# Performance work log

Measured on AMD Instinct MI355X. Metric: run time of the kernel, lower is better.

The kernel has to match this reference:

```python
import jax, jax.numpy as jnp
import numpy as np

PRE_HEIGHT = 96
PRE_WIDTH = 128


def setup_inputs() -> dict:
    key = jax.random.key(0)
    B, K, H, W = 32, 64, 96, 128
    x = jax.random.normal(key, (B, K, H, W), dtype=jnp.float32)
    return {"combined_hm_preds": x, "batch_size": B, "num_of_kp": K}


def reference(combined_hm_preds, batch_size, num_of_kp):
    B, K, H, W = combined_hm_preds.shape
    # nn.Softmax() with no dim on a 4D tensor -> softmax over dim=1 (channels)
    map_val_all = jax.nn.softmax(combined_hm_preds, axis=1)
    # zeta[b,k] = sum over spatial of the channel-softmaxed map
    get_zeta = map_val_all.sum(axis=(2, 3))  # [B, K]
    js = jnp.arange(W, dtype=map_val_all.dtype)
    iis = jnp.arange(H, dtype=map_val_all.dtype)
    # per-channel weighted coordinate sums
    Sx = jnp.einsum('bkij,j->bk', map_val_all, js)  # [B, K]
    Sy = jnp.einsum('bkij,i->bk', map_val_all, iis)  # [B, K]
    # faithful to the original: accumulators are never reset across k or b,
    # so each keypoint uses the inclusive cumulative sum in flattened (b,k) order
    cum_x = jnp.cumsum(Sx.reshape(-1)).reshape(B, K)
    cum_y = jnp.cumsum(Sy.reshape(-1)).reshape(B, K)
    kx = jnp.round(cum_x / get_zeta)
    ky = jnp.round(cum_y / get_zeta)
    # out-of-range clamp to the image center, as in the original
    kx = jnp.where((kx > PRE_WIDTH) | (kx < 0), PRE_WIDTH * 0.5, kx)
    ky = jnp.where((ky > PRE_HEIGHT) | (ky < 0), PRE_HEIGHT * 0.5, ky)
    keypoint = jnp.stack([kx, ky], axis=-1)  # [B, K, 2]
    return (map_val_all, keypoint, get_zeta)
```

## Files before the change

### kernel.cpp

```cpp
#include <hip/hip_runtime.h>
#include <math.h>

#define BB 32
#define KK 64
#define HH 96
#define WW 128
#define HW (HH*WW)
#define MAP_SIZE (BB*KK*HW)
#define NBK (BB*KK)
#define TK 64
#define NTB (HW/TK)
#define NBLK (BB*NTB)

__global__ __launch_bounds__(64, 2) void fused_k(const float* __restrict__ x,
                                                 float* __restrict__ out,
                                                 double* __restrict__ sxyz) {
    __shared__ float sm[KK][65];

    int blk  = blockIdx.x;
    int b    = blk / NTB;
    int tile = blk - b * NTB;
    int t    = threadIdx.x;
    size_t base = (size_t)b * (KK * HW) + (size_t)tile * TK + t;

    float den = 0.f;
    #pragma unroll
    for (int k = 0; k < KK; ++k) {
        float e = __expf(x[base + (size_t)k * HW]);
        sm[k][t] = e;
        den += e;
    }
    float inv = 1.f / den;

    #pragma unroll
    for (int k = 0; k < KK; ++k) {
        float m = sm[k][t] * inv;
        __builtin_nontemporal_store(m, &out[base + (size_t)k * HW]);
        sm[k][t] = m;
    }
    __syncthreads();

    float z = 0.f, sxl = 0.f;
    #pragma unroll
    for (int j = 0; j < 64; ++j) {
        float m = sm[t][j];
        z   += m;
        sxl  = fmaf(m, (float)j, sxl);
    }
    float gxb = (float)((tile & 1) << 6);
    float gy  = (float)(tile >> 1);
    int bk = b * KK + t;
    atomicAdd(&sxyz[bk * 3 + 0], (double)fmaf(gxb, z, sxl));
    atomicAdd(&sxyz[bk * 3 + 1], (double)(gy * z));
    atomicAdd(&sxyz[bk * 3 + 2], (double)z);
}

__global__ __launch_bounds__(256) void keypoint_k(const double* __restrict__ sxyz,
                                                  float* __restrict__ kp,
                                                  float* __restrict__ zeta) {
    const int PT = NBK / 256;
    int t = threadIdx.x;
    int lane = t & 63, wid = t >> 6;

    double vx[PT], vy[PT], vz[PT];
    double cx = 0.0, cy = 0.0;
    #pragma unroll
    for (int e = 0; e < PT; ++e) {
        int idx = t * PT + e;
        cx += sxyz[idx * 3 + 0]; vx[e] = cx;
        cy += sxyz[idx * 3 + 1]; vy[e] = cy;
        vz[e] = sxyz[idx * 3 + 2];
    }
    double tx = cx, ty = cy;
    for (int off = 1; off < 64; off <<= 1) {
        double ax = __shfl_up(tx, off, 64);
        double ay = __shfl_up(ty, off, 64);
        if (lane >= off) { tx += ax; ty += ay; }
    }
    __shared__ double wxs[4], wys[4];
    if (lane == 63) { wxs[wid] = tx; wys[wid] = ty; }
    __syncthreads();
    double offx = tx - cx, offy = ty - cy;
    for (int w2 = 0; w2 < wid; ++w2) { offx += wxs[w2]; offy += wys[w2]; }

    #pragma unroll
    for (int e = 0; e < PT; ++e) {
        int idx = t * PT + e;
        double zz = vz[e];
        double kx = rint((vx[e] + offx) / zz);
        double ky = rint((vy[e] + offy) / zz);
        float fkx = (float)kx, fky = (float)ky;
        if (fkx > 128.0f || fkx < 0.0f) fkx = 64.0f;
        if (fky > 96.0f  || fky < 0.0f) fky = 48.0f;
        kp[idx * 2 + 0] = fkx;
        kp[idx * 2 + 1] = fky;
        zeta[idx] = (float)zz;
    }
}

extern "C" void kernel_launch(void* const* d_in, const int* in_sizes, int n_in,
                              void* d_out, int out_size, void* d_ws, size_t ws_size,
                              hipStream_t stream) {
    const float* x = (const float*)d_in[0];
    float* out  = (float*)d_out;
    float* map  = out;
    float* kp   = out + MAP_SIZE;
    float* zeta = out + MAP_SIZE + NBK * 2;
    double* sxyz = (double*)d_ws;

    hipMemsetAsync(d_ws, 0, (size_t)NBK * 3 * sizeof(double), stream);
    fused_k   <<< NBLK, TK, 0, stream >>> (x, map, sxyz);
    keypoint_k<<< 1,    256, 0, stream >>> (sxyz, kp, zeta);
}
```

Before: 196.1 us.

## Split channel softmax into partial-denominator, inverse, and per-channel map kernels

Replaces the single transpose-through-shared-memory kernel with three passes. Partial exp sums over channel groups are written into the output buffer as scratch, reduced into an inverse denominator, and then a per-(b,k) kernel recomputes exp, writes the normalized map with float4 stores and reduces the coordinate sums with wave shuffles instead of double atomics. This trades an extra read of the input and some scratch traffic for fully coalesced vector accesses, larger blocks and no atomic contention.

```diff
diff --git a/kernel.cpp b/kernel.cpp
--- a/kernel.cpp
+++ b/kernel.cpp
@@ -8,51 +8,106 @@
 #define HW (HH*WW)
 #define MAP_SIZE (BB*KK*HW)
 #define NBK (BB*KK)
-#define TK 64
-#define NTB (HW/TK)
-#define NBLK (BB*NTB)
+#define GD 8
+#define SEC 6
 
-__global__ __launch_bounds__(64, 2) void fused_k(const float* __restrict__ x,
-                                                 float* __restrict__ out,
-                                                 double* __restrict__ sxyz) {
-    __shared__ float sm[KK][65];
+typedef float f32x4 __attribute__((ext_vector_type(4)));
 
-    int blk  = blockIdx.x;
-    int b    = blk / NTB;
-    int tile = blk - b * NTB;
-    int t    = threadIdx.x;
-    size_t base = (size_t)b * (KK * HW) + (size_t)tile * TK + t;
+__global__ __launch_bounds__(256) void den_part_k(const float* __restrict__ x,
+                                                  float* __restrict__ dpart) {
+    int blk = blockIdx.x;
+    int sec = blk % SEC;
+    int bg  = blk / SEC;
+    int g   = bg & (GD - 1);
+    int b   = bg >> 3;
+    int t   = threadIdx.x;
 
+    size_t pbase = (size_t)sec * 2048 + (size_t)t * 4;
+    f32x4 a0 = (f32x4){0.f, 0.f, 0.f, 0.f};
+    f32x4 a1 = (f32x4){0.f, 0.f, 0.f, 0.f};
+    #pragma unroll
+    for (int k = 0; k < 8; ++k) {
+        const f32x4* xp = reinterpret_cast<const f32x4*>(
+            x + (size_t)(b * KK + g * 8 + k) * HW + pbase);
+        f32x4 v0 = xp[0];
+        f32x4 v1 = xp[256];
+        a0.x += __expf(v0.x); a0.y += __expf(v0.y);
+        a0.z += __expf(v0.z); a0.w += __expf(v0.w);
+        a1.x += __expf(v1.x); a1.y += __expf(v1.y);
+        a1.z += __expf(v1.z); a1.w += __expf(v1.w);
+    }
+    f32x4* dp = reinterpret_cast<f32x4*>(
+        dpart + (size_t)(b * GD + g) * HW + pbase);
+    dp[0]   = a0;
+    dp[256] = a1;
+}
+
+__global__ __launch_bounds__(256) void inv_k(const float* __restrict__ dpart,
+                                             float* __restrict__ invd) {
+    int P = blockIdx.x * 256 + threadIdx.x;
+    int b = P / HW;
+    int p = P - b * HW;
     float den = 0.f;
     #pragma unroll
-    for (int k = 0; k < KK; ++k) {
-        float e = __expf(x[base + (size_t)k * HW]);
-        sm[k][t] = e;
-        den += e;
+    for (int g = 0; g < GD; ++g)
+        den += dpart[(size_t)(b * GD + g) * HW + p];
+    invd[P] = 1.f / den;
+}
+
+__global__ __launch_bounds__(256, 2) void map_k(const float* __restrict__ x,
+                                                const float* __restrict__ invd,
+                                                float* __restrict__ out,
+                                                double* __restrict__ sxyz) {
+    int blk = blockIdx.x;
+    int k   = blk & (KK - 1);
+    int b   = blk >> 6;
+    int t   = threadIdx.x;
+
+    const f32x4* xp = reinterpret_cast<const f32x4*>(x   + (size_t)blk * HW);
+    f32x4*       op = reinterpret_cast<f32x4*>      (out + (size_t)blk * HW);
+    const f32x4* ip = reinterpret_cast<const f32x4*>(invd + (size_t)b * HW);
+
+    float z = 0.f, w = 0.f, syw = 0.f;
+    #pragma unroll
+    for (int i = 0; i < 12; ++i) {
+        int idx = i * 256 + t;
+        f32x4 v  = xp[idx];
+        f32x4 iv = ip[idx];
+        f32x4 m;
+        m.x = __expf(v.x) * iv.x;
+        m.y = __expf(v.y) * iv.y;
+        m.z = __expf(v.z) * iv.z;
+        m.w = __expf(v.w) * iv.w;
+        __builtin_nontemporal_store(m, op + idx);
+        float s = (m.x + m.y) + (m.z + m.w);
+        z   += s;
+        w   += fmaf(3.f, m.w, fmaf(2.f, m.z, m.y));
+        syw  = fmaf(s, (float)(8 * i), syw);
     }
-    float inv = 1.f / den;
+    float gxb = (float)((t * 4) & (WW - 1));
+    float gyc = (float)(t >> 5);
+    double dz = (double)z;
+    double dx = (double)fmaf(gxb, z, w);
+    double dy = (double)fmaf(gyc, z, syw);
 
     #pragma unroll
-    for (int k = 0; k < KK; ++k) {
-        float m = sm[k][t] * inv;
-        __builtin_nontemporal_store(m, &out[base + (size_t)k * HW]);
-        sm[k][t] = m;
+    for (int off = 1; off < 64; off <<= 1) {
+        dz += __shfl_xor(dz, off, 64);
+        dx += __shfl_xor(dx, off, 64);
+        dy += __shfl_xor(dy, off, 64);
     }
+    __shared__ double wz[4], wx[4], wy[4];
+    int lane = t & 63, wid = t >> 6;
+    if (lane == 0) { wz[wid] = dz; wx[wid] = dx; wy[wid] = dy; }
     __syncthreads();
-
-    float z = 0.f, sxl = 0.f;
-    #pragma unroll
-    for (int j = 0; j < 64; ++j) {
-        float m = sm[t][j];
-        z   += m;
-        sxl  = fmaf(m, (float)j, sxl);
+    if (t == 0) {
+        double Z  = ((wz[0] + wz[1]) + wz[2]) + wz[3];
+        double SX = ((wx[0] + wx[1]) + wx[2]) + wx[3];
+        double SY = ((wy[0] + wy[1]) + wy[2]) + wy[3];
+        sxyz[blk * 3 + 0] = SX;
+        sxyz[blk * 3 + 1] = SY;
+        sxyz[blk * 3 + 2] = Z;
     }
-    float gxb = (float)((tile & 1) << 6);
-    float gy  = (float)(tile >> 1);
-    int bk = b * KK + t;
-    atomicAdd(&sxyz[bk * 3 + 0], (double)fmaf(gxb, z, sxl));
-    atomicAdd(&sxyz[bk * 3 + 1], (double)(gy * z));
-    atomicAdd(&sxyz[bk * 3 + 2], (double)z);
 }
 
 __global__ __launch_bounds__(256) void keypoint_k(const double* __restrict__ sxyz,
@@ -107,8 +162,11 @@
     float* kp   = out + MAP_SIZE;
     float* zeta = out + MAP_SIZE + NBK * 2;
     double* sxyz = (double*)d_ws;
+    float*  invd = (float*)((char*)d_ws + 65536);
+    float* dpart = map;
 
-    hipMemsetAsync(d_ws, 0, (size_t)NBK * 3 * sizeof(double), stream);
-    fused_k   <<< NBLK, TK, 0, stream >>> (x, map, sxyz);
-    keypoint_k<<< 1,    256, 0, stream >>> (sxyz, kp, zeta);
+    den_part_k<<< BB * GD * SEC, 256, 0, stream >>> (x, dpart);
+    inv_k     <<< (BB * HW) / 256, 256, 0, stream >>> (dpart, invd);
+    map_k     <<< NBK, 256, 0, stream >>> (x, invd, map, sxyz);
+    keypoint_k<<< 1,   256, 0, stream >>> (sxyz, kp, zeta);
 }
```

Result: slower. 202.4 us (+3.2%).
